# Performance work log

Hardware: AMD Instinct MI355X
Metric: run time of the kernel (lower is better)

## Reference

```python
import jax, jax.numpy as jnp
import numpy as np

N, M, D = 1024, 1024, 256

def setup_inputs() -> dict:
    key = jax.random.key(0)
    ks = jax.random.split(key, 10)
    s = 1.0 / np.sqrt(D)
    return {
        "f_r": jax.random.normal(ks[0], (N, D), jnp.float32),
        "f_r_prime": jax.random.normal(ks[1], (M, D), jnp.float32),
        "W_w": jax.random.uniform(ks[2], (D, D), jnp.float32, -s, s),
        "W_b": jax.random.uniform(ks[3], (D,), jnp.float32, -s, s),
        "Wp_w": jax.random.uniform(ks[4], (D, D), jnp.float32, -s, s),
        "Wp_b": jax.random.uniform(ks[5], (D,), jnp.float32, -s, s),
        "w_w": jax.random.uniform(ks[6], (1, D), jnp.float32, -s, s),
        "w_b": jax.random.uniform(ks[7], (1,), jnp.float32, -s, s),
        "wp_w": jax.random.uniform(ks[8], (1, D), jnp.float32, -s, s),
        "wp_b": jax.random.uniform(ks[9], (1,), jnp.float32, -s, s),
    }

def reference(f_r, f_r_prime, W_w, W_b, Wp_w, Wp_b, w_w, w_b, wp_w, wp_b):
    q = f_r @ W_w.T + W_b            # [N, D]
    k = f_r_prime @ Wp_w.T + Wp_b    # [M, D]
    # additive (Bahdanau) scores: tanh over broadcast sum [N, M, D]
    h = jnp.tanh(q[:, None, :] + k[None, :, :])
    alpha = h @ w_w.T + w_b          # [N, M, 1]
    alpha = jax.nn.softmax(alpha, axis=1)
    # stage-1 pooling over M (weights on raw f_r_prime, as in source)
    context = jnp.sum(alpha * f_r_prime[None, :, :], axis=1)  # [N, D]
    # stage-2 attention pooling over N
    alpha_p = jax.nn.softmax(context @ wp_w.T + wp_b, axis=0)  # [N, 1]
    pool = jnp.sum(alpha_p * context, axis=0, keepdims=True)   # [1, D]
    return pool
```

## Files before the change

kernel.cpp:

```cpp
#include <hip/hip_runtime.h>

#define NN 1024
#define MM 1024
#define DD 256

typedef float floatx2 __attribute__((ext_vector_type(2)));

__device__ __forceinline__ float rcp_fast(float x) { return __builtin_amdgcn_rcpf(x); }

__global__ __launch_bounds__(256) void gemm_exp_kernel(
    const float* __restrict__ f_r,  const float* __restrict__ W_w,  const float* __restrict__ W_b,
    const float* __restrict__ f_rp, const float* __restrict__ Wp_w, const float* __restrict__ Wp_b,
    float* __restrict__ Eq, float* __restrict__ EkT, float* __restrict__ out0)
{
    __shared__ float As[32][36];
    __shared__ float Bs[32][68];
    __shared__ float T[64][36];

    const int b = blockIdx.x;
    const int t = threadIdx.x;
    if (b == 0) out0[t] = 0.f;

    const int mat  = b >> 7;
    const int tile = b & 127;
    const int rt = tile & 31, dt = tile >> 5;
    const float* __restrict__ A    = mat ? f_rp : f_r;
    const float* __restrict__ B    = mat ? Wp_w : W_w;
    const float* __restrict__ bias = mat ? Wp_b : W_b;

    const int tx = t & 15, ty = t >> 4;
    const int r0 = rt * 32, d0 = dt * 64;
    const int ar = t >> 3, ak = (t & 7) * 4;
    const int br = t >> 2, bk = (t & 3) * 8;

    float acc[2][4];
    #pragma unroll
    for (int i = 0; i < 2; ++i)
        #pragma unroll
        for (int j = 0; j < 4; ++j) acc[i][j] = 0.f;

    for (int kk = 0; kk < DD; kk += 32) {
        float4 av  = *(const float4*)(A + (size_t)(r0 + ar) * DD + kk + ak);
        float4 bv0 = *(const float4*)(B + (size_t)(d0 + br) * DD + kk + bk);
        float4 bv1 = *(const float4*)(B + (size_t)(d0 + br) * DD + kk + bk + 4);
        __syncthreads();
        As[ak + 0][ar] = av.x; As[ak + 1][ar] = av.y; As[ak + 2][ar] = av.z; As[ak + 3][ar] = av.w;
        Bs[bk + 0][br] = bv0.x; Bs[bk + 1][br] = bv0.y; Bs[bk + 2][br] = bv0.z; Bs[bk + 3][br] = bv0.w;
        Bs[bk + 4][br] = bv1.x; Bs[bk + 5][br] = bv1.y; Bs[bk + 6][br] = bv1.z; Bs[bk + 7][br] = bv1.w;
        __syncthreads();
        #pragma unroll
        for (int k = 0; k < 32; ++k) {
            float2 a2 = *(const float2*)&As[k][ty * 2];
            float4 b4 = *(const float4*)&Bs[k][tx * 4];
            float aa[2] = {a2.x, a2.y};
            float bb[4] = {b4.x, b4.y, b4.z, b4.w};
            #pragma unroll
            for (int i = 0; i < 2; ++i)
                #pragma unroll
                for (int j = 0; j < 4; ++j)
                    acc[i][j] = fmaf(aa[i], bb[j], acc[i][j]);
        }
    }

    float bj[4];
    #pragma unroll
    for (int j = 0; j < 4; ++j) bj[j] = bias[d0 + tx * 4 + j];

    float e[2][4];
    #pragma unroll
    for (int i = 0; i < 2; ++i)
        #pragma unroll
        for (int j = 0; j < 4; ++j) {
            float v = acc[i][j] + bj[j];
            v = fminf(fmaxf(v, -5.f), 5.f);
            e[i][j] = __expf(2.f * v);
        }

    if (mat == 0) {
        #pragma unroll
        for (int i = 0; i < 2; ++i)
            *(float4*)&Eq[(size_t)(r0 + ty * 2 + i) * DD + d0 + tx * 4] =
                make_float4(e[i][0], e[i][1], e[i][2], e[i][3]);
    } else {
        __syncthreads();
        #pragma unroll
        for (int i = 0; i < 2; ++i)
            #pragma unroll
            for (int j = 0; j < 4; ++j) T[tx * 4 + j][ty * 2 + i] = e[i][j];
        __syncthreads();
        const int dl = t >> 3, rl = (t & 7) * 4;
        #pragma unroll
        for (int h = 0; h < 2; ++h) {
            int dloc = dl + 32 * h;
            float4 tv = *(const float4*)&T[dloc][rl];
            *(float4*)&EkT[(size_t)(d0 + dloc) * MM + r0 + rl] = tv;
        }
    }
}

__global__ __launch_bounds__(1024, 8) void fused_attn_kernel(
    const float* __restrict__ Eq, const float* __restrict__ EkT,
    const float* __restrict__ w_w, const float* __restrict__ frp,
    float* __restrict__ ctxA, float* __restrict__ ctxB,
    float* __restrict__ SpA, float* __restrict__ SpB)
{
    __shared__ __align__(16) char usm_raw[65536];
    float2 (*accbuf)[4][256] = (float2 (*)[4][256])(void*)usm_raw;
    float4 (*ctxred)[4][64]  = (float4 (*)[4][64])(void*)usm_raw;
    __shared__ float alsm[4][512];
    __shared__ float redsm[4][4];

    const int t  = threadIdx.x;
    const int tg = t >> 8;
    const int tm = t & 255;
    const int bm = blockIdx.x & 1;
    const int n0 = (blockIdx.x >> 1) * 4;
    const int m0 = bm * 512;

    const int dh = __builtin_amdgcn_readfirstlane(tg * 64);
    const float* __restrict__ eqb = Eq + (size_t)n0 * DD + dh;
    const float* __restrict__ wwb = w_w + dh;

    const floatx2 one2 = {1.f, 1.f};
    floatx2 acc2[4] = {{0.f,0.f},{0.f,0.f},{0.f,0.f},{0.f,0.f}};

    const float* ekb = EkT + (size_t)dh * MM + m0 + 2 * tm;
    float2 c0 = *(const float2*)(ekb + 0 * MM);
    float2 c1 = *(const float2*)(ekb + 1 * MM);
    float2 c2 = *(const float2*)(ekb + 2 * MM);
    float2 c3 = *(const float2*)(ekb + 3 * MM);

    for (int gi = 0; gi < 16; ++gi) {
        float2 p0 = c0, p1 = c1, p2 = c2, p3 = c3;
        if (gi < 15) {
            const float* nb = ekb + (size_t)(gi * 4 + 4) * MM;
            p0 = *(const float2*)(nb + 0 * MM);
            p1 = *(const float2*)(nb + 1 * MM);
            p2 = *(const float2*)(nb + 2 * MM);
            p3 = *(const float2*)(nb + 3 * MM);
        }
        const int db = gi * 4;
        float4 w4 = *(const float4*)(wwb + db);
        floatx2 kv0 = {c0.x, c0.y}, kv1 = {c1.x, c1.y};
        floatx2 kv2 = {c2.x, c2.y}, kv3 = {c3.x, c3.y};
        #pragma unroll
        for (int n = 0; n < 4; ++n) {
            float4 q4 = *(const float4*)(eqb + n * DD + db);
            floatx2 x0 = q4.x * kv0 + one2;
            floatx2 x1 = q4.y * kv1 + one2;
            floatx2 x2 = q4.z * kv2 + one2;
            floatx2 x3 = q4.w * kv3 + one2;
            floatx2 p01 = x0 * x1;
            floatx2 p23 = x2 * x3;
            floatx2 n01 = w4.x * x1 + w4.y * x0;
            floatx2 n23 = w4.z * x3 + w4.w * x2;
            floatx2 nc  = n01 * p23 + n23 * p01;
            floatx2 pt  = p01 * p23;
            floatx2 r;  r.x = rcp_fast(pt.x);  r.y = rcp_fast(pt.y);
            acc2[n] += nc * r;
        }
        c0 = p0; c1 = p1; c2 = p2; c3 = p3;
    }

    #pragma unroll
    for (int n = 0; n < 4; ++n)
        accbuf[tg][n][tm] = make_float2(-2.f * acc2[n].x, -2.f * acc2[n].y);
    __syncthreads();

    const int g = tg;
    const int w4id = (t >> 6) & 3;
    const int lane = t & 63;
    float2 a0 = accbuf[0][g][tm], a1 = accbuf[1][g][tm];
    float2 a2 = accbuf[2][g][tm], a3 = accbuf[3][g][tm];
    float sx = a0.x + a1.x + a2.x + a3.x;
    float sy = a0.y + a1.y + a2.y + a3.y;
    float ex = __expf(sx), ey = __expf(sy);
    *(float2*)&alsm[g][2 * tm] = make_float2(ex, ey);
    float sm = ex + ey;
    #pragma unroll
    for (int off = 32; off > 0; off >>= 1) sm += __shfl_xor(sm, off);
    if (lane == 0) redsm[g][w4id] = sm;
    __syncthreads();
    if (tm == 0) {
        float* Sp = bm ? SpB : SpA;
        Sp[n0 + g] = redsm[g][0] + redsm[g][1] + redsm[g][2] + redsm[g][3];
    }

    const int cc = t & 63;
    const int rr = t >> 6;
    floatx2 axl[4] = {{0.f,0.f},{0.f,0.f},{0.f,0.f},{0.f,0.f}};
    floatx2 axh[4] = {{0.f,0.f},{0.f,0.f},{0.f,0.f},{0.f,0.f}};
    const float* fb = frp + (size_t)(m0 + rr * 32) * DD + 4 * cc;
    for (int m8 = 0; m8 < 8; ++m8) {
        float alv[4][4];
        #pragma unroll
        for (int n = 0; n < 4; ++n) {
            float4 a4 = *(const float4*)&alsm[n][rr * 32 + m8 * 4];
            alv[n][0] = a4.x; alv[n][1] = a4.y; alv[n][2] = a4.z; alv[n][3] = a4.w;
        }
        #pragma unroll
        for (int mm = 0; mm < 4; ++mm) {
            float4 f = *(const float4*)(fb + (size_t)(m8 * 4 + mm) * DD);
            floatx2 fl = {f.x, f.y}, fh = {f.z, f.w};
            #pragma unroll
            for (int n = 0; n < 4; ++n) {
                axl[n] += alv[n][mm] * fl;
                axh[n] += alv[n][mm] * fh;
            }
        }
    }
    #pragma unroll
    for (int n = 0; n < 4; ++n)
        ctxred[rr][n][cc] = make_float4(axl[n].x, axl[n].y, axh[n].x, axh[n].y);
    __syncthreads();

    const int nn = t >> 8, d = t & 255;
    float s = 0.f;
    #pragma unroll
    for (int r = 0; r < 16; ++r)
        s += ((const float*)&ctxred[r][nn][d >> 2])[d & 3];
    float* ctxP = bm ? ctxB : ctxA;
    ctxP[(size_t)(n0 + nn) * DD + d] = s;
}

__global__ __launch_bounds__(256) void combine_kernel(
    const float* __restrict__ ctxA, const float* __restrict__ ctxB,
    const float* __restrict__ SpA, const float* __restrict__ SpB,
    const float* __restrict__ wp_w,
    float* __restrict__ ctx, float* __restrict__ score)
{
    const int t = threadIdx.x, lane = t & 63;
    const int row = blockIdx.x * 4 + (t >> 6);
    const float inv = rcp_fast(SpA[row] + SpB[row]);
    const size_t off = (size_t)row * DD + 4 * lane;
    float4 a = *(const float4*)(ctxA + off);
    float4 b = *(const float4*)(ctxB + off);
    float4 c = make_float4((a.x + b.x) * inv, (a.y + b.y) * inv,
                           (a.z + b.z) * inv, (a.w + b.w) * inv);
    *(float4*)(ctx + off) = c;
    float4 w = *(const float4*)(wp_w + 4 * lane);
    float p = c.x * w.x + c.y * w.y + c.z * w.z + c.w * w.w;
    #pragma unroll
    for (int o = 32; o > 0; o >>= 1) p += __shfl_xor(p, o);
    if (lane == 0) score[row] = p;
}

__global__ __launch_bounds__(256) void pool_kernel(
    const float* __restrict__ ctx, const float* __restrict__ score,
    float* __restrict__ out)
{
    __shared__ float red[8];
    const int t = threadIdx.x, lane = t & 63, wid = t >> 6;
    const int n0 = blockIdx.x * 4;

    float s0 = score[t], s1 = score[t + 256], s2 = score[t + 512], s3 = score[t + 768];
    float mx = fmaxf(fmaxf(s0, s1), fmaxf(s2, s3));
    #pragma unroll
    for (int off = 32; off > 0; off >>= 1) mx = fmaxf(mx, __shfl_xor(mx, off));
    if (lane == 0) red[wid] = mx;
    __syncthreads();
    mx = fmaxf(fmaxf(red[0], red[1]), fmaxf(red[2], red[3]));

    float se = __expf(s0 - mx) + __expf(s1 - mx) + __expf(s2 - mx) + __expf(s3 - mx);
    #pragma unroll
    for (int off = 32; off > 0; off >>= 1) se += __shfl_xor(se, off);
    if (lane == 0) red[4 + wid] = se;
    __syncthreads();
    se = red[4] + red[5] + red[6] + red[7];
    float invS = rcp_fast(se);

    float r = 0.f;
    #pragma unroll
    for (int i = 0; i < 4; ++i) {
        float ap = __expf(score[n0 + i] - mx) * invS;
        r = fmaf(ap, ctx[(size_t)(n0 + i) * DD + t], r);
    }
    atomicAdd(out + t, r);
}

extern "C" void kernel_launch(void* const* d_in, const int* in_sizes, int n_in,
                              void* d_out, int out_size, void* d_ws, size_t ws_size,
                              hipStream_t stream) {
    const float* f_r  = (const float*)d_in[0];
    const float* f_rp = (const float*)d_in[1];
    const float* W_w  = (const float*)d_in[2];
    const float* W_b  = (const float*)d_in[3];
    const float* Wp_w = (const float*)d_in[4];
    const float* Wp_b = (const float*)d_in[5];
    const float* w_w  = (const float*)d_in[6];
    const float* wp_w = (const float*)d_in[8];
    float* out = (float*)d_out;

    float* ws    = (float*)d_ws;
    float* Eq    = ws;
    float* EkT   = ws + 262144;
    float* ctxA  = ws + 524288;
    float* ctxB  = ws + 786432;
    float* ctxn  = ws + 1048576;
    float* SpA   = ws + 1310720;
    float* SpB   = ws + 1311744;
    float* score = ws + 1312768;

    gemm_exp_kernel<<<256, 256, 0, stream>>>(f_r, W_w, W_b, f_rp, Wp_w, Wp_b, Eq, EkT, out);
    fused_attn_kernel<<<512, 1024, 0, stream>>>(Eq, EkT, w_w, f_rp, ctxA, ctxB, SpA, SpB);
    combine_kernel<<<256, 256, 0, stream>>>(ctxA, ctxB, SpA, SpB, wp_w, ctxn, score);
    pool_kernel<<<256, 256, 0, stream>>>(ctxn, score, out);
}
```

Measured before the change: 127.6 us.

## Split fused attention into score and context kernels, fold combine into context

The fused attention kernel is split in two. A score kernel (512 threads, two D-halves of 128) computes the exp scores, writes the full N×M score matrix to global memory and stores per-half row sums. A context kernel then covers all M per block of 4 rows, normalises, and computes the stage-2 score, which removes the separate combine kernel and the ctxA/ctxB partials. In exchange, the 4 MB score matrix now makes a round trip through global memory, and the score kernel has fewer threads per block, with each thread doing twice as much work.

```diff
diff --git a/kernel.cpp b/kernel.cpp
--- a/kernel.cpp
+++ b/kernel.cpp
@@ -98,41 +98,38 @@
     }
 }
 
-__global__ __launch_bounds__(1024, 8) void fused_attn_kernel(
+__global__ __launch_bounds__(512, 8) void score_kernel(
     const float* __restrict__ Eq, const float* __restrict__ EkT,
-    const float* __restrict__ w_w, const float* __restrict__ frp,
-    float* __restrict__ ctxA, float* __restrict__ ctxB,
-    float* __restrict__ SpA, float* __restrict__ SpB)
+    const float* __restrict__ w_w,
+    float* __restrict__ E, float* __restrict__ Sp2)
 {
-    __shared__ __align__(16) char usm_raw[65536];
-    float2 (*accbuf)[4][256] = (float2 (*)[4][256])(void*)usm_raw;
-    float4 (*ctxred)[4][64]  = (float4 (*)[4][64])(void*)usm_raw;
-    __shared__ float alsm[4][512];
-    __shared__ float redsm[4][4];
+    __shared__ float2 part[2][4][256];
+    __shared__ float wred[4][4];
 
     const int t  = threadIdx.x;
-    const int tg = t >> 8;
+    const int dh = t >> 8;
     const int tm = t & 255;
+    const int ng = blockIdx.x >> 1;
     const int bm = blockIdx.x & 1;
-    const int n0 = (blockIdx.x >> 1) * 4;
+    const int n0 = ng * 4;
     const int m0 = bm * 512;
 
-    const int dh = __builtin_amdgcn_readfirstlane(tg * 64);
-    const float* __restrict__ eqb = Eq + (size_t)n0 * DD + dh;
-    const float* __restrict__ wwb = w_w + dh;
+    const int dbase = __builtin_amdgcn_readfirstlane(dh * 128);
+    const float* __restrict__ eqb = Eq + (size_t)n0 * DD + dbase;
+    const float* __restrict__ wwb = w_w + dbase;
+    const float* __restrict__ ekb = EkT + (size_t)dbase * MM + m0 + 2 * tm;
 
     const floatx2 one2 = {1.f, 1.f};
-    floatx2 acc2[4] = {{0.f,0.f},{0.f,0.f},{0.f,0.f},{0.f,0.f}};
-
-    const float* ekb = EkT + (size_t)dh * MM + m0 + 2 * tm;
+    floatx2 acc[4] = {{0.f,0.f},{0.f,0.f},{0.f,0.f},{0.f,0.f}};
+
     float2 c0 = *(const float2*)(ekb + 0 * MM);
     float2 c1 = *(const float2*)(ekb + 1 * MM);
     float2 c2 = *(const float2*)(ekb + 2 * MM);
     float2 c3 = *(const float2*)(ekb + 3 * MM);
 
-    for (int gi = 0; gi < 16; ++gi) {
+    for (int gi = 0; gi < 32; ++gi) {
         float2 p0 = c0, p1 = c1, p2 = c2, p3 = c3;
-        if (gi < 15) {
+        if (gi < 31) {
             const float* nb = ekb + (size_t)(gi * 4 + 4) * MM;
             p0 = *(const float2*)(nb + 0 * MM);
             p1 = *(const float2*)(nb + 1 * MM);
@@ -157,50 +154,67 @@
             floatx2 nc  = n01 * p23 + n23 * p01;
             floatx2 pt  = p01 * p23;
             floatx2 r;  r.x = rcp_fast(pt.x);  r.y = rcp_fast(pt.y);
-            acc2[n] += nc * r;
+            acc[n] += nc * r;
         }
         c0 = p0; c1 = p1; c2 = p2; c3 = p3;
     }
 
     #pragma unroll
     for (int n = 0; n < 4; ++n)
-        accbuf[tg][n][tm] = make_float2(-2.f * acc2[n].x, -2.f * acc2[n].y);
-    __syncthreads();
-
-    const int g = tg;
-    const int w4id = (t >> 6) & 3;
+        part[dh][n][tm] = make_float2(acc[n].x, acc[n].y);
+    __syncthreads();
+
     const int lane = t & 63;
-    float2 a0 = accbuf[0][g][tm], a1 = accbuf[1][g][tm];
-    float2 a2 = accbuf[2][g][tm], a3 = accbuf[3][g][tm];
-    float sx = a0.x + a1.x + a2.x + a3.x;
-    float sy = a0.y + a1.y + a2.y + a3.y;
-    float ex = __expf(sx), ey = __expf(sy);
-    *(float2*)&alsm[g][2 * tm] = make_float2(ex, ey);
-    float sm = ex + ey;
-    #pragma unroll
-    for (int off = 32; off > 0; off >>= 1) sm += __shfl_xor(sm, off);
-    if (lane == 0) redsm[g][w4id] = sm;
-    __syncthreads();
-    if (tm == 0) {
-        float* Sp = bm ? SpB : SpA;
-        Sp[n0 + g] = redsm[g][0] + redsm[g][1] + redsm[g][2] + redsm[g][3];
-    }
-
+    if (t < 256) {
+        #pragma unroll
+        for (int n = 0; n < 4; ++n) {
+            float2 a = part[0][n][t];
+            float2 b = part[1][n][t];
+            float ex = __expf(-2.f * (a.x + b.x));
+            float ey = __expf(-2.f * (a.y + b.y));
+            *(float2*)&E[(size_t)(n0 + n) * MM + m0 + 2 * t] = make_float2(ex, ey);
+            float sm = ex + ey;
+            #pragma unroll
+            for (int off = 32; off > 0; off >>= 1) sm += __shfl_xor(sm, off);
+            if (lane == 0) wred[n][t >> 6] = sm;
+        }
+    }
+    __syncthreads();
+    if (t < 4)
+        Sp2[(size_t)(n0 + t) * 2 + bm] =
+            wred[t][0] + wred[t][1] + wred[t][2] + wred[t][3];
+}
+
+__global__ __launch_bounds__(1024, 8) void ctx_kernel(
+    const float* __restrict__ E, const float* __restrict__ frp,
+    const float* __restrict__ Sp2, const float* __restrict__ wp_w,
+    float* __restrict__ ctx, float* __restrict__ score)
+{
+    __shared__ float4 ctxred[16][4][64];
+    __shared__ float redsc[16];
+
+    const int t = threadIdx.x;
+    const int n0 = blockIdx.x * 4;
     const int cc = t & 63;
-    const int rr = t >> 6;
+    const int lane = t & 63;
+    const int rr = __builtin_amdgcn_readfirstlane(t >> 6);
+    const int m0 = rr * 64;
+
     floatx2 axl[4] = {{0.f,0.f},{0.f,0.f},{0.f,0.f},{0.f,0.f}};
     floatx2 axh[4] = {{0.f,0.f},{0.f,0.f},{0.f,0.f},{0.f,0.f}};
-    const float* fb = frp + (size_t)(m0 + rr * 32) * DD + 4 * cc;
-    for (int m8 = 0; m8 < 8; ++m8) {
+    const float* fb = frp + (size_t)m0 * DD + 4 * cc;
+    const float* eb = E + (size_t)n0 * MM + m0;
+
+    for (int m4 = 0; m4 < 16; ++m4) {
         float alv[4][4];
         #pragma unroll
         for (int n = 0; n < 4; ++n) {
-            float4 a4 = *(const float4*)&alsm[n][rr * 32 + m8 * 4];
+            float4 a4 = *(const float4*)(eb + (size_t)n * MM + m4 * 4);
             alv[n][0] = a4.x; alv[n][1] = a4.y; alv[n][2] = a4.z; alv[n][3] = a4.w;
         }
         #pragma unroll
         for (int mm = 0; mm < 4; ++mm) {
-            float4 f = *(const float4*)(fb + (size_t)(m8 * 4 + mm) * DD);
+            float4 f = *(const float4*)(fb + (size_t)(m4 * 4 + mm) * DD);
             floatx2 fl = {f.x, f.y}, fh = {f.z, f.w};
             #pragma unroll
             for (int n = 0; n < 4; ++n) {
@@ -214,35 +228,24 @@
         ctxred[rr][n][cc] = make_float4(axl[n].x, axl[n].y, axh[n].x, axh[n].y);
     __syncthreads();
 
-    const int nn = t >> 8, d = t & 255;
+    const int nn = __builtin_amdgcn_readfirstlane(t >> 8);
+    const int d = t & 255;
     float s = 0.f;
     #pragma unroll
     for (int r = 0; r < 16; ++r)
         s += ((const float*)&ctxred[r][nn][d >> 2])[d & 3];
-    float* ctxP = bm ? ctxB : ctxA;
-    ctxP[(size_t)(n0 + nn) * DD + d] = s;
-}
-
-__global__ __launch_bounds__(256) void combine_kernel(
-    const float* __restrict__ ctxA, const float* __restrict__ ctxB,
-    const float* __restrict__ SpA, const float* __restrict__ SpB,
-    const float* __restrict__ wp_w,
-    float* __restrict__ ctx, float* __restrict__ score)
-{
-    const int t = threadIdx.x, lane = t & 63;
-    const int row = blockIdx.x * 4 + (t >> 6);
-    const float inv = rcp_fast(SpA[row] + SpB[row]);
-    const size_t off = (size_t)row * DD + 4 * lane;
-    float4 a = *(const float4*)(ctxA + off);
-    float4 b = *(const float4*)(ctxB + off);
-    float4 c = make_float4((a.x + b.x) * inv, (a.y + b.y) * inv,
-                           (a.z + b.z) * inv, (a.w + b.w) * inv);
-    *(float4*)(ctx + off) = c;
-    float4 w = *(const float4*)(wp_w + 4 * lane);
-    float p = c.x * w.x + c.y * w.y + c.z * w.z + c.w * w.w;
-    #pragma unroll
-    for (int o = 32; o > 0; o >>= 1) p += __shfl_xor(p, o);
-    if (lane == 0) score[row] = p;
+    const int row = n0 + nn;
+    const float S = Sp2[(size_t)row * 2 + 0] + Sp2[(size_t)row * 2 + 1];
+    float sn = s * rcp_fast(S);
+    ctx[(size_t)row * DD + d] = sn;
+
+    float p = sn * wp_w[d];
+    #pragma unroll
+    for (int off = 32; off > 0; off >>= 1) p += __shfl_xor(p, off);
+    if (lane == 0) redsc[t >> 6] = p;
+    __syncthreads();
+    if (t < 4)
+        score[n0 + t] = redsc[4 * t] + redsc[4 * t + 1] + redsc[4 * t + 2] + redsc[4 * t + 3];
 }
 
 __global__ __launch_bounds__(256) void pool_kernel(
@@ -294,15 +297,13 @@
     float* ws    = (float*)d_ws;
     float* Eq    = ws;
     float* EkT   = ws + 262144;
-    float* ctxA  = ws + 524288;
-    float* ctxB  = ws + 786432;
-    float* ctxn  = ws + 1048576;
-    float* SpA   = ws + 1310720;
-    float* SpB   = ws + 1311744;
-    float* score = ws + 1312768;
+    float* E     = ws + 524288;
+    float* ctx   = ws + 1572864;
+    float* Sp2   = ws + 1835008;
+    float* score = ws + 1837056;
 
     gemm_exp_kernel<<<256, 256, 0, stream>>>(f_r, W_w, W_b, f_rp, Wp_w, Wp_b, Eq, EkT, out);
-    fused_attn_kernel<<<512, 1024, 0, stream>>>(Eq, EkT, w_w, f_rp, ctxA, ctxB, SpA, SpB);
-    combine_kernel<<<256, 256, 0, stream>>>(ctxA, ctxB, SpA, SpB, wp_w, ctxn, score);
-    pool_kernel<<<256, 256, 0, stream>>>(ctxn, score, out);
-}
+    score_kernel<<<512, 512, 0, stream>>>(Eq, EkT, w_w, E, Sp2);
+    ctx_kernel<<<256, 1024, 0, stream>>>(E, f_rp, Sp2, wp_w, ctx, score);
+    pool_kernel<<<256, 256, 0, stream>>>(ctx, score, out);
+}
```

Measured after the change: 131.9 us. +3.4%, slower.
